# Kernel tuning notes

Measured on AMD Instinct MI355X. Metric: run time of the kernel, lower is better.

## Reference

```python
import jax, jax.numpy as jnp
import numpy as np

DIM = 768
NUM_HEADS = 16
HEAD_DIM = DIM // NUM_HEADS  # 48


def setup_inputs() -> dict:
    key = jax.random.key(0)
    ks = jax.random.split(key, 9)
    s = 1.0 / np.sqrt(DIM)
    return {
        "x": jax.random.normal(ks[0], (4, 2048, DIM), dtype=jnp.float32),
        "Wq": jax.random.uniform(ks[1], (DIM, DIM), jnp.float32, -s, s),
        "bq": jax.random.uniform(ks[2], (DIM,), jnp.float32, -s, s),
        "Wk": jax.random.uniform(ks[3], (DIM, DIM), jnp.float32, -s, s),
        "bk": jax.random.uniform(ks[4], (DIM,), jnp.float32, -s, s),
        "Wv": jax.random.uniform(ks[5], (DIM, DIM), jnp.float32, -s, s),
        "bv": jax.random.uniform(ks[6], (DIM,), jnp.float32, -s, s),
        "Wo": jax.random.uniform(ks[7], (DIM, DIM), jnp.float32, -s, s),
        "bo": jax.random.uniform(ks[8], (DIM,), jnp.float32, -s, s),
    }


def reference(x, Wq, bq, Wk, bk, Wv, bv, Wo, bo):
    B, S, D = x.shape
    H, Dh = NUM_HEADS, HEAD_DIM
    # qkv projections -> [B, H, S, Dh]
    q = (x @ Wq.T + bq).reshape(B, S, H, Dh).transpose(0, 2, 1, 3)
    k = (x @ Wk.T + bk).reshape(B, S, H, Dh).transpose(0, 2, 1, 3)
    v = (x @ Wv.T + bv).reshape(B, S, H, Dh).transpose(0, 2, 1, 3)
    scale = 1.0 / np.sqrt(Dh).astype(np.float32)
    scores = jnp.einsum('bhqd,bhkd->bhqk', q, k) * scale  # [B,H,S,S]
    attn = jax.nn.softmax(scores, axis=-1)
    # dropout is identity in eval mode
    out = jnp.einsum('bhqk,bhkd->bhqd', attn, v)  # [B,H,S,Dh]
    out = out.transpose(0, 2, 1, 3).reshape(B, S, D)
    return out @ Wo.T + bo
```

## Files before the change

kernel.cpp:

```cpp
#include <hip/hip_runtime.h>
#include <cstdint>
#include <cstddef>


typedef short s8v __attribute__((ext_vector_type(8)));
typedef float f4v __attribute__((ext_vector_type(4)));
typedef float f16v __attribute__((ext_vector_type(16)));

static constexpr int Bn = 4, Sn = 2048, Dn = 768, Hn = 16, DhN = 48, Dp = 64;
static constexpr int MS = Bn * Sn;

#define MFMA16(a, b, c) __builtin_amdgcn_mfma_f32_16x16x32_bf16((a), (b), (c), 0, 0, 0)
#define MFMA32(a, b, c) __builtin_amdgcn_mfma_f32_32x32x16_bf16((a), (b), (c), 0, 0, 0)

__device__ __forceinline__ int swz4(int r) { return (r + (r >> 2)) & 3; }

__device__ __forceinline__ ushort f2b(float f) {
  return (ushort)((__builtin_bit_cast(uint32_t, f) + 0x8000u) >> 16);
}
__device__ __forceinline__ uint32_t packbf(float a, float b) {
  uint32_t ua = __builtin_bit_cast(uint32_t, a) + 0x8000u;
  uint32_t ub = __builtin_bit_cast(uint32_t, b) + 0x8000u;
  return __builtin_amdgcn_perm(ub, ua, 0x07060302u);
}
__device__ __forceinline__ float fexp2(float x) {
  return __builtin_amdgcn_exp2f(x);
}
__device__ __forceinline__ void gload_lds16(const ushort* g, ushort* l) {
  __builtin_amdgcn_global_load_lds(
      (const __attribute__((address_space(1))) uint32_t*)g,
      (__attribute__((address_space(3))) uint32_t*)l, 16, 0, 0);
}

__global__ void cvt_all(const float* __restrict__ x,
                        const float* __restrict__ wq, const float* __restrict__ wk,
                        const float* __restrict__ wv, const float* __restrict__ wo,
                        ushort* __restrict__ xb, ushort* __restrict__ wqkv,
                        ushort* __restrict__ wob) {
  const int bid = blockIdx.x;
  const float* src;
  ushort* dst;
  int i;
  if (bid < 6144) {
    src = x; dst = xb; i = bid * 256 + threadIdx.x;
  } else {
    const int r = (bid - 6144) / 576;
    i = ((bid - 6144) % 576) * 256 + threadIdx.x;
    src = (r == 0) ? wq : (r == 1) ? wk : (r == 2) ? wv : wo;
    dst = (r < 3) ? (wqkv + (size_t)r * Dn * Dn) : wob;
  }
  float4 f = ((const float4*)src)[i];
  ushort4 o = { f2b(f.x), f2b(f.y), f2b(f.z), f2b(f.w) };
  ((ushort4*)dst)[i] = o;
}

__global__ __launch_bounds__(256) void gemm_qkv(
    const ushort* __restrict__ A, const ushort* __restrict__ W,
    const float* __restrict__ bq, const float* __restrict__ bk, const float* __restrict__ bv,
    ushort* __restrict__ outq, ushort* __restrict__ outk, ushort* __restrict__ outv,
    float qscale) {
  __shared__ __align__(16) ushort As[128][32];
  __shared__ __align__(16) ushort Bs[128][32];
  const int tid = threadIdx.x, lane = tid & 63, wave = tid >> 6;
  const int l15 = lane & 15, g = lane >> 4;
  const int m0 = blockIdx.y * 128, n0 = blockIdx.x * 128;
  const int wqm = (wave >> 1) * 64;
  const int wqx = (wave & 1) * 64;
  f4v acc[4][4] = {};

  const int slot0 = wave * 128 + lane;
  const int slot1 = slot0 + 64;
  const int r0 = slot0 >> 2, u0 = ((slot0 & 3) ^ swz4(r0 & 15)) * 8;
  const int r1 = slot1 >> 2, u1 = ((slot1 & 3) ^ swz4(r1 & 15)) * 8;
  const ushort* ag0 = A + (size_t)(m0 + r0) * Dn + u0;
  const ushort* ag1 = A + (size_t)(m0 + r1) * Dn + u1;
  const ushort* bg0 = W + (size_t)(n0 + r0) * Dn + u0;
  const ushort* bg1 = W + (size_t)(n0 + r1) * Dn + u1;
  ushort* lA0 = &As[0][0] + slot0 * 8;
  ushort* lA1 = &As[0][0] + slot1 * 8;
  ushort* lB0 = &Bs[0][0] + slot0 * 8;
  ushort* lB1 = &Bs[0][0] + slot1 * 8;
  const int fcol = (g ^ swz4(l15)) * 8;

  for (int k0 = 0; k0 < Dn; k0 += 32) {
    __syncthreads();
    gload_lds16(ag0 + k0, lA0);
    gload_lds16(ag1 + k0, lA1);
    gload_lds16(bg0 + k0, lB0);
    gload_lds16(bg1 + k0, lB1);
    __syncthreads();
    s8v wf[4], xf[4];
#pragma unroll
    for (int i = 0; i < 4; ++i) wf[i] = *(const s8v*)&Bs[wqm + i * 16 + l15][fcol];
#pragma unroll
    for (int j = 0; j < 4; ++j) xf[j] = *(const s8v*)&As[wqx + j * 16 + l15][fcol];
#pragma unroll
    for (int i = 0; i < 4; ++i)
#pragma unroll
      for (int j = 0; j < 4; ++j) acc[i][j] = MFMA16(wf[i], xf[j], acc[i][j]);
  }

  const int region = blockIdx.x / 6;
  const int nbase = n0 - region * 768;
  const float* bias = (region == 0) ? bq : (region == 1) ? bk : bv;
#pragma unroll
  for (int i = 0; i < 4; ++i) {
    const int n = nbase + wqm + i * 16 + g * 4;
    const float4 b4 = *(const float4*)&bias[n];
    const int h = n / DhN, dh = n - h * DhN;
#pragma unroll
    for (int j = 0; j < 4; ++j) {
      const int s = m0 + wqx + j * 16 + l15;
      const int b = s >> 11, srow = s & 2047;
      const int bh = b * Hn + h;
      float v0 = acc[i][j][0] + b4.x, v1 = acc[i][j][1] + b4.y;
      float v2 = acc[i][j][2] + b4.z, v3 = acc[i][j][3] + b4.w;
      if (region == 0) { v0 *= qscale; v1 *= qscale; v2 *= qscale; v3 *= qscale; }
      if (region < 2) {
        ushort4 o = { f2b(v0), f2b(v1), f2b(v2), f2b(v3) };
        ushort* dst = region ? outk : outq;
        *(ushort4*)&dst[((size_t)bh * Sn + srow) * Dp + dh] = o;
      } else {
        outv[((size_t)bh * DhN + dh + 0) * Sn + srow] = f2b(v0);
        outv[((size_t)bh * DhN + dh + 1) * Sn + srow] = f2b(v1);
        outv[((size_t)bh * DhN + dh + 2) * Sn + srow] = f2b(v2);
        outv[((size_t)bh * DhN + dh + 3) * Sn + srow] = f2b(v3);
      }
    }
  }
}

__global__ __launch_bounds__(256) void gemm_out(
    const ushort* __restrict__ A, const ushort* __restrict__ W,
    const float* __restrict__ bias, float* __restrict__ out) {
  __shared__ __align__(16) ushort As[128][32];
  __shared__ __align__(16) ushort Bs[128][32];
  const int tid = threadIdx.x, lane = tid & 63, wave = tid >> 6;
  const int l15 = lane & 15, g = lane >> 4;
  const int m0 = blockIdx.y * 128, n0 = blockIdx.x * 128;
  const int wqm = (wave >> 1) * 64;
  const int wqx = (wave & 1) * 64;
  f4v acc[4][4] = {};

  const int slot0 = wave * 128 + lane;
  const int slot1 = slot0 + 64;
  const int r0 = slot0 >> 2, u0 = ((slot0 & 3) ^ swz4(r0 & 15)) * 8;
  const int r1 = slot1 >> 2, u1 = ((slot1 & 3) ^ swz4(r1 & 15)) * 8;
  const ushort* ag0 = A + (size_t)(m0 + r0) * Dn + u0;
  const ushort* ag1 = A + (size_t)(m0 + r1) * Dn + u1;
  const ushort* bg0 = W + (size_t)(n0 + r0) * Dn + u0;
  const ushort* bg1 = W + (size_t)(n0 + r1) * Dn + u1;
  ushort* lA0 = &As[0][0] + slot0 * 8;
  ushort* lA1 = &As[0][0] + slot1 * 8;
  ushort* lB0 = &Bs[0][0] + slot0 * 8;
  ushort* lB1 = &Bs[0][0] + slot1 * 8;
  const int fcol = (g ^ swz4(l15)) * 8;

  for (int k0 = 0; k0 < Dn; k0 += 32) {
    __syncthreads();
    gload_lds16(ag0 + k0, lA0);
    gload_lds16(ag1 + k0, lA1);
    gload_lds16(bg0 + k0, lB0);
    gload_lds16(bg1 + k0, lB1);
    __syncthreads();
    s8v wf[4], xf[4];
#pragma unroll
    for (int i = 0; i < 4; ++i) wf[i] = *(const s8v*)&Bs[wqm + i * 16 + l15][fcol];
#pragma unroll
    for (int j = 0; j < 4; ++j) xf[j] = *(const s8v*)&As[wqx + j * 16 + l15][fcol];
#pragma unroll
    for (int i = 0; i < 4; ++i)
#pragma unroll
      for (int j = 0; j < 4; ++j) acc[i][j] = MFMA16(wf[i], xf[j], acc[i][j]);
  }

#pragma unroll
  for (int i = 0; i < 4; ++i) {
    const int n = n0 + wqm + i * 16 + g * 4;
    const float4 b4 = *(const float4*)&bias[n];
#pragma unroll
    for (int j = 0; j < 4; ++j) {
      const int s = m0 + wqx + j * 16 + l15;
      float4 o4 = { acc[i][j][0] + b4.x, acc[i][j][1] + b4.y,
                    acc[i][j][2] + b4.z, acc[i][j][3] + b4.w };
      *(float4*)&out[(size_t)s * Dn + n] = o4;
    }
  }
}

__global__ __launch_bounds__(256) void attn_kernel(
    const ushort* __restrict__ qg, const ushort* __restrict__ kg,
    const ushort* __restrict__ vg, ushort* __restrict__ og) {
  __shared__ __align__(16) ushort Ka[64][32];
  __shared__ __align__(16) ushort Kb[64][16];
  __shared__ __align__(16) ushort Vs[64][64];
  const int tid = threadIdx.x;
  const int lane = tid & 63;
  const int wave = tid >> 6;
  const int l31 = lane & 31;
  const int h = lane >> 5;
  const int bh = blockIdx.y;
  const int q0 = blockIdx.x * 128;
  const ushort* qb = qg + (size_t)bh * Sn * Dp;
  const ushort* kb = kg + (size_t)bh * Sn * Dp;
  const ushort* vb = vg + (size_t)bh * DhN * Sn;

#pragma unroll
  for (int t = 0; t < 2; ++t) {
    const int idx = tid + t * 256;
    const int row = 48 + (idx >> 5);
    ((uint32_t*)&Vs[row][0])[idx & 31] = (row == 48) ? 0x3F803F80u : 0u;
  }

  s8v qf[3];
#pragma unroll
  for (int kc = 0; kc < 3; ++kc)
    qf[kc] = *(const s8v*)(qb + (size_t)(q0 + wave * 32 + l31) * Dp + kc * 16 + h * 8);

  const ushort* gsrc[3];
  ushort* ldst[3];
  int gstep[3];
#pragma unroll
  for (int t = 0; t < 3; ++t) {
    const int c = wave + 4 * t;
    if (c < 4) {
      const int row = 16 * c + (lane >> 2), j = lane & 3;
      gsrc[t] = kb + (size_t)row * Dp + (j ^ ((row >> 1) & 3)) * 8;
      ldst[t] = &Ka[0][0] + 16 * c * 32 + lane * 8;
      gstep[t] = 64 * Dp;
    } else if (c < 6) {
      const int row = 32 * (c - 4) + (lane >> 1), j = lane & 1;
      gsrc[t] = kb + (size_t)row * Dp + 32 + (j ^ ((row >> 2) & 1)) * 8;
      ldst[t] = &Kb[0][0] + 32 * (c - 4) * 16 + lane * 8;
      gstep[t] = 64 * Dp;
    } else {
      const int row = 8 * (c - 6) + (lane >> 3), j = lane & 7;
      gsrc[t] = vb + (size_t)row * Sn + (j ^ (row & 7)) * 8;
      ldst[t] = &Vs[0][0] + 8 * (c - 6) * 64 + lane * 8;
      gstep[t] = 64;
    }
  }

  f16v o0 = {}, o1 = {};

  for (int kt = 0; kt < Sn; kt += 64) {
    __syncthreads();
#pragma unroll
    for (int t = 0; t < 3; ++t) {
      gload_lds16(gsrc[t], ldst[t]);
      gsrc[t] += gstep[t];
    }
    __syncthreads();

#pragma unroll
    for (int mg = 0; mg < 2; ++mg) {
      const int row = 32 * mg + l31;
      const int s1 = (l31 >> 1) & 3, s2 = (l31 >> 2) & 1;
      s8v a0 = *(const s8v*)&Ka[row][((0 | h) ^ s1) * 8];
      s8v a1 = *(const s8v*)&Ka[row][((2 | h) ^ s1) * 8];
      s8v a2 = *(const s8v*)&Kb[row][((h) ^ s2) * 8];
      f16v sc = {};
      sc = MFMA32(a0, qf[0], sc);
      sc = MFMA32(a1, qf[1], sc);
      sc = MFMA32(a2, qf[2], sc);
      float p[16];
#pragma unroll
      for (int r = 0; r < 16; ++r) p[r] = fexp2(sc[r]);

#pragma unroll
      for (int c2 = 0; c2 < 2; ++c2) {
        const int rb = 8 * c2;
        const uint32_t lo0 = packbf(p[rb + 0], p[rb + 1]);
        const uint32_t lo1 = packbf(p[rb + 2], p[rb + 3]);
        const uint32_t hi0 = packbf(p[rb + 4], p[rb + 5]);
        const uint32_t hi1 = packbf(p[rb + 6], p[rb + 7]);
        const uint32_t t0 = __shfl_xor(h ? lo0 : hi0, 32, 64);
        const uint32_t t1 = __shfl_xor(h ? lo1 : hi1, 32, 64);
        uint4 af;
        af.x = h ? t0 : lo0;
        af.y = h ? t1 : lo1;
        af.z = h ? hi0 : t0;
        af.w = h ? hi1 : t1;
        const s8v pa = __builtin_bit_cast(s8v, af);
        const int kcv = 2 * mg + c2;
        const int vc = ((2 * kcv + h) ^ (l31 & 7)) * 8;
        const s8v v0 = *(const s8v*)&Vs[l31][vc];
        const s8v v1 = *(const s8v*)&Vs[32 + l31][vc];
        o0 = MFMA32(pa, v0, o0);
        o1 = MFMA32(pa, v1, o1);
      }
    }
  }

  const int b = bh >> 4, hh = bh & 15;
#pragma unroll
  for (int r = 0; r < 16; ++r) {
    const int q = (r & 3) + 8 * (r >> 2) + 4 * h;
    const float lsum = __shfl(o1[r], 16 + (lane & 32), 64);
    const float inv = 1.0f / lsum;
    const int s = q0 + wave * 32 + q;
    const size_t base = ((size_t)(b * Sn + s)) * Dn + hh * DhN;
    og[base + l31] = f2b(o0[r] * inv);
    if (l31 < 16) og[base + 32 + l31] = f2b(o1[r] * inv);
  }
}

extern "C" void kernel_launch(void* const* d_in, const int* in_sizes, int n_in,
                              void* d_out, int out_size, void* d_ws, size_t ws_size,
                              hipStream_t stream) {
  (void)in_sizes; (void)n_in; (void)out_size; (void)ws_size;
  const float* x  = (const float*)d_in[0];
  const float* Wq = (const float*)d_in[1];
  const float* bq = (const float*)d_in[2];
  const float* Wk = (const float*)d_in[3];
  const float* bk = (const float*)d_in[4];
  const float* Wv = (const float*)d_in[5];
  const float* bv = (const float*)d_in[6];
  const float* Wo = (const float*)d_in[7];
  const float* bo = (const float*)d_in[8];

  size_t off = 0;
  auto alloc = [&](size_t bytes) {
    void* p = (char*)d_ws + off;
    off += (bytes + 255) & ~(size_t)255;
    return p;
  };
  ushort* xb    = (ushort*)alloc((size_t)MS * Dn * 2);
  ushort* Wqkvb = (ushort*)alloc((size_t)3 * Dn * Dn * 2);
  ushort* Wob   = (ushort*)alloc((size_t)Dn * Dn * 2);
  ushort* qbuf  = (ushort*)alloc((size_t)Bn * Hn * Sn * Dp * 2);
  ushort* kbuf  = (ushort*)alloc((size_t)Bn * Hn * Sn * Dp * 2);
  ushort* vbuf  = (ushort*)alloc((size_t)Bn * Hn * DhN * Sn * 2);
  ushort* ao    = (ushort*)alloc((size_t)MS * Dn * 2);

  cvt_all<<<6144 + 4 * 576, 256, 0, stream>>>(x, Wq, Wk, Wv, Wo, xb, Wqkvb, Wob);

  const dim3 blk(256);
  const float qscale = 0.20823510929813633f;
  gemm_qkv<<<dim3(18, MS / 128), blk, 0, stream>>>(xb, Wqkvb, bq, bk, bv,
                                                   qbuf, kbuf, vbuf, qscale);

  attn_kernel<<<dim3(Sn / 128, Bn * Hn), blk, 0, stream>>>(qbuf, kbuf, vbuf, ao);

  gemm_out<<<dim3(6, MS / 128), blk, 0, stream>>>(ao, Wob, bo, (float*)d_out);
}
```

Baseline: 253.0 us.

## Double-buffer K/V LDS tiles in attention and raise MFMA wave priority

```diff
diff --git a/kernel.cpp b/kernel.cpp
--- a/kernel.cpp
+++ b/kernel.cpp
@@ -191,9 +191,9 @@
 __global__ __launch_bounds__(256) void attn_kernel(
     const ushort* __restrict__ qg, const ushort* __restrict__ kg,
     const ushort* __restrict__ vg, ushort* __restrict__ og) {
-  __shared__ __align__(16) ushort Ka[64][32];
-  __shared__ __align__(16) ushort Kb[64][16];
-  __shared__ __align__(16) ushort Vs[64][64];
+  __shared__ __align__(16) ushort Ka[2][64][32];
+  __shared__ __align__(16) ushort Kb[2][64][16];
+  __shared__ __align__(16) ushort Vs[2][64][64];
   const int tid = threadIdx.x;
   const int lane = tid & 63;
   const int wave = tid >> 6;
@@ -206,11 +206,13 @@
   const ushort* vb = vg + (size_t)bh * DhN * Sn;
 
 #pragma unroll
-  for (int t = 0; t < 2; ++t) {
-    const int idx = tid + t * 256;
-    const int row = 48 + (idx >> 5);
-    ((uint32_t*)&Vs[row][0])[idx & 31] = (row == 48) ? 0x3F803F80u : 0u;
-  }
+  for (int d = 0; d < 2; ++d)
+#pragma unroll
+    for (int t = 0; t < 2; ++t) {
+      const int idx = tid + t * 256;
+      const int row = 48 + (idx >> 5);
+      ((uint32_t*)&Vs[d][row][0])[idx & 31] = (row == 48) ? 0x3F803F80u : 0u;
+    }
 
   s8v qf[3];
 #pragma unroll
@@ -218,7 +220,8 @@
     qf[kc] = *(const s8v*)(qb + (size_t)(q0 + wave * 32 + l31) * Dp + kc * 16 + h * 8);
 
   const ushort* gsrc[3];
-  ushort* ldst[3];
+  ushort* ldst0[3];
+  ushort* ldst1[3];
   int gstep[3];
 #pragma unroll
   for (int t = 0; t < 3; ++t) {
@@ -226,43 +229,59 @@
     if (c < 4) {
       const int row = 16 * c + (lane >> 2), j = lane & 3;
       gsrc[t] = kb + (size_t)row * Dp + (j ^ ((row >> 1) & 3)) * 8;
-      ldst[t] = &Ka[0][0] + 16 * c * 32 + lane * 8;
+      ldst0[t] = &Ka[0][0][0] + 16 * c * 32 + lane * 8;
+      ldst1[t] = ldst0[t] + 64 * 32;
       gstep[t] = 64 * Dp;
     } else if (c < 6) {
       const int row = 32 * (c - 4) + (lane >> 1), j = lane & 1;
       gsrc[t] = kb + (size_t)row * Dp + 32 + (j ^ ((row >> 2) & 1)) * 8;
-      ldst[t] = &Kb[0][0] + 32 * (c - 4) * 16 + lane * 8;
+      ldst0[t] = &Kb[0][0][0] + 32 * (c - 4) * 16 + lane * 8;
+      ldst1[t] = ldst0[t] + 64 * 16;
       gstep[t] = 64 * Dp;
     } else {
       const int row = 8 * (c - 6) + (lane >> 3), j = lane & 7;
       gsrc[t] = vb + (size_t)row * Sn + (j ^ (row & 7)) * 8;
-      ldst[t] = &Vs[0][0] + 8 * (c - 6) * 64 + lane * 8;
+      ldst0[t] = &Vs[0][0][0] + 8 * (c - 6) * 64 + lane * 8;
+      ldst1[t] = ldst0[t] + 64 * 64;
       gstep[t] = 64;
     }
   }
 
   f16v o0 = {}, o1 = {};
 
+#pragma unroll
+  for (int t = 0; t < 3; ++t) {
+    gload_lds16(gsrc[t], ldst0[t]);
+    gsrc[t] += gstep[t];
+  }
+  __syncthreads();
+
+  int cur = 0;
   for (int kt = 0; kt < Sn; kt += 64) {
-    __syncthreads();
-#pragma unroll
-    for (int t = 0; t < 3; ++t) {
-      gload_lds16(gsrc[t], ldst[t]);
-      gsrc[t] += gstep[t];
-    }
-    __syncthreads();
+    if (kt < Sn - 64) {
+#pragma unroll
+      for (int t = 0; t < 3; ++t) {
+        gload_lds16(gsrc[t], cur ? ldst0[t] : ldst1[t]);
+        gsrc[t] += gstep[t];
+      }
+    }
+    const ushort(*KaC)[32] = Ka[cur];
+    const ushort(*KbC)[16] = Kb[cur];
+    const ushort(*VsC)[64] = Vs[cur];
 
 #pragma unroll
     for (int mg = 0; mg < 2; ++mg) {
       const int row = 32 * mg + l31;
       const int s1 = (l31 >> 1) & 3, s2 = (l31 >> 2) & 1;
-      s8v a0 = *(const s8v*)&Ka[row][((0 | h) ^ s1) * 8];
-      s8v a1 = *(const s8v*)&Ka[row][((2 | h) ^ s1) * 8];
-      s8v a2 = *(const s8v*)&Kb[row][((h) ^ s2) * 8];
+      s8v a0 = *(const s8v*)&KaC[row][((0 | h) ^ s1) * 8];
+      s8v a1 = *(const s8v*)&KaC[row][((2 | h) ^ s1) * 8];
+      s8v a2 = *(const s8v*)&KbC[row][((h) ^ s2) * 8];
       f16v sc = {};
+      __builtin_amdgcn_s_setprio(1);
       sc = MFMA32(a0, qf[0], sc);
       sc = MFMA32(a1, qf[1], sc);
       sc = MFMA32(a2, qf[2], sc);
+      __builtin_amdgcn_s_setprio(0);
       float p[16];
 #pragma unroll
       for (int r = 0; r < 16; ++r) p[r] = fexp2(sc[r]);
@@ -284,12 +303,16 @@
         const s8v pa = __builtin_bit_cast(s8v, af);
         const int kcv = 2 * mg + c2;
         const int vc = ((2 * kcv + h) ^ (l31 & 7)) * 8;
-        const s8v v0 = *(const s8v*)&Vs[l31][vc];
-        const s8v v1 = *(const s8v*)&Vs[32 + l31][vc];
+        const s8v v0 = *(const s8v*)&VsC[l31][vc];
+        const s8v v1 = *(const s8v*)&VsC[32 + l31][vc];
+        __builtin_amdgcn_s_setprio(1);
         o0 = MFMA32(pa, v0, o0);
         o1 = MFMA32(pa, v1, o1);
+        __builtin_amdgcn_s_setprio(0);
       }
     }
+    __syncthreads();
+    cur ^= 1;
   }
 
   const int b = bh >> 4, hh = bh & 15;
```

After: 254.2 us. About the same (+0.5%).
